# Performance work log

Measured on AMD Instinct MI355X. Metric: run time of the kernel, lower is better.

The kernel has to match this reference:

```python
import jax, jax.numpy as jnp
import numpy as np

B, N, T, D = 8, 32, 64, 128
E, H = 4, 32  # edge_dim, hidden_edge


def setup_inputs() -> dict:
    key = jax.random.key(0)
    ks = jax.random.split(key, 12)
    s = 1.0 / np.sqrt(D)
    inp = {
        "x": jax.random.normal(ks[0], (B, N, T, D), jnp.float32),
        "edge_features": jax.random.normal(ks[1], (B * T, N, N, E), jnp.float32),
        "A_prior": jax.random.uniform(ks[2], (B * T, N, N, 5), jnp.float32),
        "entity_padding_mask": jnp.zeros((B, N), bool),
        "Wq": jax.random.normal(ks[3], (D, D), jnp.float32) * s,
        "Wk": jax.random.normal(ks[4], (D, D), jnp.float32) * s,
        "Wv": jax.random.normal(ks[5], (D, D), jnp.float32) * s,
        "Theta": jax.random.normal(ks[6], (D, D), jnp.float32) * s,
        "W_fuse": jax.random.normal(ks[7], (1, 5), jnp.float32) * 0.4,
        "W1": jax.random.normal(ks[8], (H, 2 * D + E), jnp.float32) * (1.0 / np.sqrt(2 * D + E)),
        "b1": jnp.zeros((H,), jnp.float32),
        "W2": jax.random.normal(ks[9], (1, H), jnp.float32) * (1.0 / np.sqrt(H)),
        "b2": jnp.zeros((1,), jnp.float32),
        "gamma": jnp.ones((D,), jnp.float32),
        "beta": jnp.zeros((D,), jnp.float32),
        "phys_weight": jnp.array(1.0, jnp.float32),
        "prior_weight": jnp.array(1.0, jnp.float32),
    }
    return inp


def reference(x, edge_features, A_prior, entity_padding_mask, Wq, Wk, Wv, Theta,
              W_fuse, W1, b1, W2, b2, gamma, beta, phys_weight, prior_weight):
    b, n, t, d = x.shape
    BT = b * t
    Z = x.transpose(0, 2, 1, 3).reshape(BT, n, d)          # (BT, N, D)
    Q = Z @ Wq.T
    K = Z @ Wk.T
    V = Z @ Wv.T
    content = jnp.einsum('bnd,bmd->bnm', Q, K) / np.sqrt(d)
    # edge MLP: first linear decomposed over the concat [Qi, Kj, edge_features]
    W1q, W1k, W1e = W1[:, :d], W1[:, d:2 * d], W1[:, 2 * d:]
    hq = Q @ W1q.T                                          # (BT, N, H)
    hk = K @ W1k.T                                          # (BT, N, H)
    he = edge_features @ W1e.T                              # (BT, N, N, H)
    h = jax.nn.relu(hq[:, :, None, :] + hk[:, None, :, :] + he + b1)
    phys = (h @ W2.T)[..., 0] + b2[0]                       # (BT, N, N)
    logits = content + phys_weight * phys
    # prior fusion
    prior = (A_prior @ W_fuse.T)[..., 0]                    # (BT, N, N)
    prior = jnp.clip(jnp.nan_to_num(prior, nan=0.0, posinf=0.0, neginf=0.0), 0.0)
    logits = logits + prior_weight * jnp.log(prior + 1e-6)
    # padding mask
    mask_bt = jnp.broadcast_to(entity_padding_mask[:, None, :], (b, t, n)).reshape(BT, n)
    invalid = mask_bt[:, :, None] | mask_bt[:, None, :]
    logits = jnp.where(invalid, -1e9, logits)
    alpha = jax.nn.softmax(logits, axis=-1)
    spatial = jnp.einsum('bnm,bmd->bnd', alpha, V)
    out_f = (spatial @ Theta.T).reshape(b, t, n, d)
    y = Z.reshape(b, t, n, d) + out_f
    mu = y.mean(-1, keepdims=True)
    var = y.var(-1, keepdims=True)
    y = (y - mu) / jnp.sqrt(var + 1e-5) * gamma + beta      # LayerNorm
    out = y.transpose(0, 2, 1, 3)                           # (B, N, T, D)
    out = jnp.where(entity_padding_mask[:, :, None, None], 0.0, out)
    return out
```

## Files before the change

### kernel.cpp

```cpp
#include <hip/hip_runtime.h>


typedef __bf16 bf16x8 __attribute__((ext_vector_type(8)));
typedef float  f32x4  __attribute__((ext_vector_type(4)));

static __device__ __forceinline__ unsigned short f2bf(float f) {
    unsigned u = __float_as_uint(f);
    u += 0x7fffu + ((u >> 16) & 1u);
    return (unsigned short)(u >> 16);
}
static __device__ __forceinline__ float bf2f(unsigned short u) {
    return __uint_as_float(((unsigned)u) << 16);
}
static __device__ __forceinline__ unsigned pack2(float a, float b) {
    return (unsigned)f2bf(a) | ((unsigned)f2bf(b) << 16);
}


__global__ __launch_bounds__(256) void k0_prep(
    const float* __restrict__ Wq, const float* __restrict__ Wk,
    const float* __restrict__ Wv, const float* __restrict__ Theta,
    const float* __restrict__ W1, unsigned short* __restrict__ Wfrag)
{
    const int tid = threadIdx.x;
    if (blockIdx.x < 32) {
        int gid = blockIdx.x * 256 + tid;
        int g = gid >> 11, c = gid & 2047;
        int ntk = c >> 6, lane = c & 63;
        int i = (ntk >> 2) * 16 + (lane & 15);
        int j = (ntk & 3) * 32 + (lane >> 4) * 8;
        const float* src = (g == 0 ? Wq : g == 1 ? Wk : g == 2 ? Wv : Theta) + (size_t)i * 128 + j;
        float4 a = *(const float4*)(src);
        float4 b = *(const float4*)(src + 4);
        uint4 pk;
        pk.x = pack2(a.x, a.y); pk.y = pack2(a.z, a.w);
        pk.z = pack2(b.x, b.y); pk.w = pack2(b.z, b.w);
        *(uint4*)(Wfrag + (size_t)gid * 8) = pk;
    } else {
        int b2 = blockIdx.x - 32;
        int mat = b2 & 1;
        int hbase = (b2 >> 1) * 2;
        int hl = tid >> 7, col = tid & 127;
        int h = hbase + hl;
        const float* Wsel = mat ? Wk : Wq;
        const float* w1r = W1 + (size_t)h * 260 + mat * 128;
        float acc = 0.f;
        for (int i = 0; i < 128; ++i)
            acc = fmaf(w1r[i], Wsel[(size_t)i * 128 + col], acc);
        int nt = h >> 4;
        unsigned base = 65536u + (unsigned)mat * 4096u;
        int lane = (h & 15) | (((col >> 3) & 3) << 4);
        int ks = col >> 5, vj = col & 7;
        Wfrag[base + (unsigned)((nt * 4 + ks) * 64 + lane) * 8 + vj] = f2bf(acc);
    }
}

__global__ __launch_bounds__(256, 2)
void gnn_all(const float* __restrict__ x, const float* __restrict__ edge,
             const float* __restrict__ A_prior, const unsigned char* __restrict__ pad_mask,
             const unsigned short* __restrict__ Wfrag, const float* __restrict__ Wfuse,
             const float* __restrict__ W1, const float* __restrict__ b1,
             const float* __restrict__ W2, const float* __restrict__ b2,
             const float* __restrict__ gma, const float* __restrict__ bta,
             const float* __restrict__ physw, const float* __restrict__ priorw,
             float* __restrict__ out)
{
    __shared__ __align__(16) unsigned char arena[52224];
    float*          Qs    = (float*)arena;
    unsigned short* Zfrag = (unsigned short*)arena;
    float*          ThOut = Qs;
    float*          Ks    = (float*)(arena + 16896);
    unsigned short* Sfrag = (unsigned short*)(arena + 16896);
    unsigned short* Vs    = (unsigned short*)(arena + 33792);
    float*          Lg    = (float*)(arena + 42496);
    unsigned short* hqL   = (unsigned short*)(arena + 47104);
    unsigned short* hkL   = (unsigned short*)(arena + 49280);
    float4*         W1e_s = (float4*)(arena + 51456);
    float*          W2_s  = (float*)(arena + 51968);
    float*          maskrow = (float*)(arena + 52096);

    const int tid = threadIdx.x;
    const int bt  = blockIdx.x;
    const int b_  = bt >> 6, t_ = bt & 63;

    const float pw  = physw[0];
    const float rw_ = priorw[0];
    const float b2v = b2[0];
    const float wf0 = Wfuse[0], wf1 = Wfuse[1], wf2 = Wfuse[2],
                wf3 = Wfuse[3], wf4 = Wfuse[4];

    const int wv = tid >> 6, lane = tid & 63;
    const int quad = lane >> 4, col0 = lane & 15;
    const float b1lo = b1[col0], b1hi = b1[16 + col0];
    const int d0p = (tid & 31) * 4, ngp = tid >> 5;
    const float4 g4  = *(const float4*)(gma + d0p);
    const float4 be4 = *(const float4*)(bta + d0p);

    const int mp = tid & 15, npg = tid >> 4;
    const int n0 = npg * 2, mA = mp, mB = mp + 16;
    float4 e00, e01, e10, e11;
    float  prv00, prv01, prv10, prv11;
    {
        const size_t rowA0 = ((size_t)bt * 32 + n0) * 32;
        const size_t rowA1 = ((size_t)bt * 32 + n0 + 1) * 32;
        e00 = *(const float4*)(edge + (rowA0 + mA) * 4);
        e01 = *(const float4*)(edge + (rowA0 + mB) * 4);
        e10 = *(const float4*)(edge + (rowA1 + mA) * 4);
        e11 = *(const float4*)(edge + (rowA1 + mB) * 4);
        const float* p00 = A_prior + (rowA0 + mA) * 5;
        const float* p01 = A_prior + (rowA0 + mB) * 5;
        const float* p10 = A_prior + (rowA1 + mA) * 5;
        const float* p11 = A_prior + (rowA1 + mB) * 5;
        float q00 = p00[0]*wf0 + p00[1]*wf1 + p00[2]*wf2 + p00[3]*wf3 + p00[4]*wf4;
        float q01 = p01[0]*wf0 + p01[1]*wf1 + p01[2]*wf2 + p01[3]*wf3 + p01[4]*wf4;
        float q10 = p10[0]*wf0 + p10[1]*wf1 + p10[2]*wf2 + p10[3]*wf3 + p10[4]*wf4;
        float q11 = p11[0]*wf0 + p11[1]*wf1 + p11[2]*wf2 + p11[3]*wf3 + p11[4]*wf4;
        if (!(fabsf(q00) < 1e30f)) q00 = 0.f;
        if (!(fabsf(q01) < 1e30f)) q01 = 0.f;
        if (!(fabsf(q10) < 1e30f)) q10 = 0.f;
        if (!(fabsf(q11) < 1e30f)) q11 = 0.f;
        prv00 = rw_ * __logf(fmaxf(q00, 0.f) + 1e-6f);
        prv01 = rw_ * __logf(fmaxf(q01, 0.f) + 1e-6f);
        prv10 = rw_ * __logf(fmaxf(q10, 0.f) + 1e-6f);
        prv11 = rw_ * __logf(fmaxf(q11, 0.f) + 1e-6f);
    }

    if (tid < 32) {
        W1e_s[tid] = *(const float4*)(W1 + (size_t)tid * 260 + 256);
        W2_s[tid]  = W2[tid];
        maskrow[tid] = pad_mask[b_ * 32 + tid] ? 1.f : 0.f;
    }

#pragma unroll
    for (int it2 = 0; it2 < 2; ++it2) {
        int f = tid + 256 * it2;
        int lane9 = f & 63, tk = f >> 6;
        int nl = (tk >> 2) * 16 + (lane9 & 15);
        int d  = (tk & 3) * 32 + (lane9 >> 4) * 8;
        const float* xr = x + ((size_t)((b_ * 32 + nl) * 64 + t_)) * 128 + d;
        float4 a = *(const float4*)(xr);
        float4 b = *(const float4*)(xr + 4);
        uint4 pk;
        pk.x = pack2(a.x, a.y); pk.y = pack2(a.z, a.w);
        pk.z = pack2(b.x, b.y); pk.w = pack2(b.z, b.w);
        *(uint4*)(Zfrag + f * 8) = pk;
    }
    __syncthreads();

    bf16x8 az00 = *(const bf16x8*)(Zfrag + ((0 * 4 + 0) * 64 + lane) * 8);
    bf16x8 az01 = *(const bf16x8*)(Zfrag + ((0 * 4 + 1) * 64 + lane) * 8);
    bf16x8 az02 = *(const bf16x8*)(Zfrag + ((0 * 4 + 2) * 64 + lane) * 8);
    bf16x8 az03 = *(const bf16x8*)(Zfrag + ((0 * 4 + 3) * 64 + lane) * 8);
    bf16x8 az10 = *(const bf16x8*)(Zfrag + ((1 * 4 + 0) * 64 + lane) * 8);
    bf16x8 az11 = *(const bf16x8*)(Zfrag + ((1 * 4 + 1) * 64 + lane) * 8);
    bf16x8 az12 = *(const bf16x8*)(Zfrag + ((1 * 4 + 2) * 64 + lane) * 8);
    bf16x8 az13 = *(const bf16x8*)(Zfrag + ((1 * 4 + 3) * 64 + lane) * 8);
    __syncthreads();

    const bf16x8* WfG = (const bf16x8*)Wfrag;
    const f32x4 zero = {0.f, 0.f, 0.f, 0.f};

#pragma unroll
    for (int k7 = 0; k7 < 7; ++k7) {
        const int nt = wv + k7 * 4;
        const int cb = ((nt < 24) ? nt * 256 : 8192 + (nt - 24) * 256) + lane;
        bf16x8 bw0 = WfG[cb];
        bf16x8 bw1 = WfG[cb + 64];
        bf16x8 bw2 = WfG[cb + 128];
        bf16x8 bw3 = WfG[cb + 192];
        f32x4 acc0 = zero, acc1 = zero;
        acc0 = __builtin_amdgcn_mfma_f32_16x16x32_bf16(az00, bw0, acc0, 0, 0, 0);
        acc1 = __builtin_amdgcn_mfma_f32_16x16x32_bf16(az10, bw0, acc1, 0, 0, 0);
        acc0 = __builtin_amdgcn_mfma_f32_16x16x32_bf16(az01, bw1, acc0, 0, 0, 0);
        acc1 = __builtin_amdgcn_mfma_f32_16x16x32_bf16(az11, bw1, acc1, 0, 0, 0);
        acc0 = __builtin_amdgcn_mfma_f32_16x16x32_bf16(az02, bw2, acc0, 0, 0, 0);
        acc1 = __builtin_amdgcn_mfma_f32_16x16x32_bf16(az12, bw2, acc1, 0, 0, 0);
        acc0 = __builtin_amdgcn_mfma_f32_16x16x32_bf16(az03, bw3, acc0, 0, 0, 0);
        acc1 = __builtin_amdgcn_mfma_f32_16x16x32_bf16(az13, bw3, acc1, 0, 0, 0);
#pragma unroll
        for (int tg = 0; tg < 2; ++tg) {
            const f32x4 acc = tg ? acc1 : acc0;
            const int tokb = tg * 16 + quad * 4;
#pragma unroll
            for (int reg = 0; reg < 4; ++reg) {
                int tok = tokb + reg;
                float v = acc[reg];
                if (nt < 8)       Qs[tok * 132 + nt * 16 + col0] = v;
                else if (nt < 16) Ks[tok * 132 + (nt - 8) * 16 + col0] = v;
                else if (nt < 24) Vs[tok * 136 + (nt - 16) * 16 + col0] = f2bf(v);
                else if (nt < 26) hqL[tok * 34 + (nt - 24) * 16 + col0] = f2bf(v + (nt == 24 ? b1lo : b1hi));
                else              hkL[tok * 34 + (nt - 26) * 16 + col0] = f2bf(v);
            }
        }
    }
    __syncthreads();

    {
        const float* qa = Qs + n0 * 132;
        const float* qb = qa + 132;
        const float* ka = Ks + mA * 132;
        const float* kb = Ks + mB * 132;
        float a00 = 0.f, a01 = 0.f, a10 = 0.f, a11 = 0.f;
        for (int j = 0; j < 128; j += 4) {
            float4 kva = *(const float4*)(ka + j);
            float4 kvb = *(const float4*)(kb + j);
            float4 qva = *(const float4*)(qa + j);
            float4 qvb = *(const float4*)(qb + j);
            a00 = fmaf(qva.x, kva.x, fmaf(qva.y, kva.y, fmaf(qva.z, kva.z, fmaf(qva.w, kva.w, a00))));
            a01 = fmaf(qva.x, kvb.x, fmaf(qva.y, kvb.y, fmaf(qva.z, kvb.z, fmaf(qva.w, kvb.w, a01))));
            a10 = fmaf(qvb.x, kva.x, fmaf(qvb.y, kva.y, fmaf(qvb.z, kva.z, fmaf(qvb.w, kva.w, a10))));
            a11 = fmaf(qvb.x, kvb.x, fmaf(qvb.y, kvb.y, fmaf(qvb.z, kvb.z, fmaf(qvb.w, kvb.w, a11))));
        }
        float pc00 = 0.f, pc01 = 0.f, pc10 = 0.f, pc11 = 0.f;
#pragma unroll
        for (int h = 0; h < 32; ++h) {
            float4 we = W1e_s[h];
            float w2v = W2_s[h];
            float hq0 = bf2f(hqL[n0 * 34 + h]);
            float hq1 = bf2f(hqL[(n0 + 1) * 34 + h]);
            float hkA = bf2f(hkL[mA * 34 + h]);
            float hkB = bf2f(hkL[mB * 34 + h]);
            float heA0 = fmaf(e00.x, we.x, fmaf(e00.y, we.y, fmaf(e00.z, we.z, e00.w * we.w)));
            float heB0 = fmaf(e01.x, we.x, fmaf(e01.y, we.y, fmaf(e01.z, we.z, e01.w * we.w)));
            float heA1 = fmaf(e10.x, we.x, fmaf(e10.y, we.y, fmaf(e10.z, we.z, e10.w * we.w)));
            float heB1 = fmaf(e11.x, we.x, fmaf(e11.y, we.y, fmaf(e11.z, we.z, e11.w * we.w)));
            pc00 = fmaf(fmaxf(hq0 + hkA + heA0, 0.f), w2v, pc00);
            pc01 = fmaf(fmaxf(hq0 + hkB + heB0, 0.f), w2v, pc01);
            pc10 = fmaf(fmaxf(hq1 + hkA + heA1, 0.f), w2v, pc10);
            pc11 = fmaf(fmaxf(hq1 + hkB + heB1, 0.f), w2v, pc11);
        }
        const float SC = 0.08838834764831845f;
        float lg00 = a00 * SC + pw * (pc00 + b2v) + prv00;
        float lg01 = a01 * SC + pw * (pc01 + b2v) + prv01;
        float lg10 = a10 * SC + pw * (pc10 + b2v) + prv10;
        float lg11 = a11 * SC + pw * (pc11 + b2v) + prv11;
        float mr0 = maskrow[n0], mr1 = maskrow[n0 + 1];
        float mcA = maskrow[mA], mcB = maskrow[mB];
        if (mr0 != 0.f || mcA != 0.f) lg00 = -1e9f;
        if (mr0 != 0.f || mcB != 0.f) lg01 = -1e9f;
        if (mr1 != 0.f || mcA != 0.f) lg10 = -1e9f;
        if (mr1 != 0.f || mcB != 0.f) lg11 = -1e9f;
        {
            float mx = fmaxf(lg00, lg01);
#pragma unroll
            for (int off = 1; off < 16; off <<= 1)
                mx = fmaxf(mx, __shfl_xor(mx, off, 64));
            float ea = __expf(lg00 - mx);
            float eb = __expf(lg01 - mx);
            float s = ea + eb;
#pragma unroll
            for (int off = 1; off < 16; off <<= 1)
                s += __shfl_xor(s, off, 64);
            float inv = 1.f / s;
            Lg[n0 * 36 + mA] = ea * inv;
            Lg[n0 * 36 + mB] = eb * inv;
        }
        {
            float mx = fmaxf(lg10, lg11);
#pragma unroll
            for (int off = 1; off < 16; off <<= 1)
                mx = fmaxf(mx, __shfl_xor(mx, off, 64));
            float ea = __expf(lg10 - mx);
            float eb = __expf(lg11 - mx);
            float s = ea + eb;
#pragma unroll
            for (int off = 1; off < 16; off <<= 1)
                s += __shfl_xor(s, off, 64);
            float inv = 1.f / s;
            Lg[(n0 + 1) * 36 + mA] = ea * inv;
            Lg[(n0 + 1) * 36 + mB] = eb * inv;
        }
    }
    __syncthreads();

    const int rg = wv & 1, ch = wv >> 1;

    {
        const int vks = d0p >> 5, vq = (d0p >> 3) & 3, vj = d0p & 7;
        const int rb = ngp * 4;
        float s00=0.f,s01=0.f,s02=0.f,s03=0.f;
        float s10=0.f,s11=0.f,s12=0.f,s13=0.f;
        float s20=0.f,s21=0.f,s22=0.f,s23=0.f;
        float s30=0.f,s31=0.f,s32=0.f,s33=0.f;
        for (int m = 0; m < 32; m += 4) {
            float4 t0 = *(const float4*)(Lg + (rb + 0) * 36 + m);
            float4 t1 = *(const float4*)(Lg + (rb + 1) * 36 + m);
            float4 t2 = *(const float4*)(Lg + (rb + 2) * 36 + m);
            float4 t3 = *(const float4*)(Lg + (rb + 3) * 36 + m);
            uint2 w0 = *(const uint2*)(Vs + (m + 0) * 136 + d0p);
            uint2 w1 = *(const uint2*)(Vs + (m + 1) * 136 + d0p);
            uint2 w2 = *(const uint2*)(Vs + (m + 2) * 136 + d0p);
            uint2 w3 = *(const uint2*)(Vs + (m + 3) * 136 + d0p);
            {
                float v0 = bf2f((unsigned short)(w0.x & 0xffffu));
                float v1 = bf2f((unsigned short)(w0.x >> 16));
                float v2 = bf2f((unsigned short)(w0.y & 0xffffu));
                float v3 = bf2f((unsigned short)(w0.y >> 16));
                s00=fmaf(t0.x,v0,s00); s01=fmaf(t0.x,v1,s01); s02=fmaf(t0.x,v2,s02); s03=fmaf(t0.x,v3,s03);
                s10=fmaf(t1.x,v0,s10); s11=fmaf(t1.x,v1,s11); s12=fmaf(t1.x,v2,s12); s13=fmaf(t1.x,v3,s13);
                s20=fmaf(t2.x,v0,s20); s21=fmaf(t2.x,v1,s21); s22=fmaf(t2.x,v2,s22); s23=fmaf(t2.x,v3,s23);
                s30=fmaf(t3.x,v0,s30); s31=fmaf(t3.x,v1,s31); s32=fmaf(t3.x,v2,s32); s33=fmaf(t3.x,v3,s33);
            }
            {
                float v0 = bf2f((unsigned short)(w1.x & 0xffffu));
                float v1 = bf2f((unsigned short)(w1.x >> 16));
                float v2 = bf2f((unsigned short)(w1.y & 0xffffu));
                float v3 = bf2f((unsigned short)(w1.y >> 16));
                s00=fmaf(t0.y,v0,s00); s01=fmaf(t0.y,v1,s01); s02=fmaf(t0.y,v2,s02); s03=fmaf(t0.y,v3,s03);
                s10=fmaf(t1.y,v0,s10); s11=fmaf(t1.y,v1,s11); s12=fmaf(t1.y,v2,s12); s13=fmaf(t1.y,v3,s13);
                s20=fmaf(t2.y,v0,s20); s21=fmaf(t2.y,v1,s21); s22=fmaf(t2.y,v2,s22); s23=fmaf(t2.y,v3,s23);
                s30=fmaf(t3.y,v0,s30); s31=fmaf(t3.y,v1,s31); s32=fmaf(t3.y,v2,s32); s33=fmaf(t3.y,v3,s33);
            }
            {
                float v0 = bf2f((unsigned short)(w2.x & 0xffffu));
                float v1 = bf2f((unsigned short)(w2.x >> 16));
                float v2 = bf2f((unsigned short)(w2.y & 0xffffu));
                float v3 = bf2f((unsigned short)(w2.y >> 16));
                s00=fmaf(t0.z,v0,s00); s01=fmaf(t0.z,v1,s01); s02=fmaf(t0.z,v2,s02); s03=fmaf(t0.z,v3,s03);
                s10=fmaf(t1.z,v0,s10); s11=fmaf(t1.z,v1,s11); s12=fmaf(t1.z,v2,s12); s13=fmaf(t1.z,v3,s13);
                s20=fmaf(t2.z,v0,s20); s21=fmaf(t2.z,v1,s21); s22=fmaf(t2.z,v2,s22); s23=fmaf(t2.z,v3,s23);
                s30=fmaf(t3.z,v0,s30); s31=fmaf(t3.z,v1,s31); s32=fmaf(t3.z,v2,s32); s33=fmaf(t3.z,v3,s33);
            }
            {
                float v0 = bf2f((unsigned short)(w3.x & 0xffffu));
                float v1 = bf2f((unsigned short)(w3.x >> 16));
                float v2 = bf2f((unsigned short)(w3.y & 0xffffu));
                float v3 = bf2f((unsigned short)(w3.y >> 16));
                s00=fmaf(t0.w,v0,s00); s01=fmaf(t0.w,v1,s01); s02=fmaf(t0.w,v2,s02); s03=fmaf(t0.w,v3,s03);
                s10=fmaf(t1.w,v0,s10); s11=fmaf(t1.w,v1,s11); s12=fmaf(t1.w,v2,s12); s13=fmaf(t1.w,v3,s13);
                s20=fmaf(t2.w,v0,s20); s21=fmaf(t2.w,v1,s21); s22=fmaf(t2.w,v2,s22); s23=fmaf(t2.w,v3,s23);
                s30=fmaf(t3.w,v0,s30); s31=fmaf(t3.w,v1,s31); s32=fmaf(t3.w,v2,s32); s33=fmaf(t3.w,v3,s33);
            }
        }
        {
            int nloc = rb + 0; int tg = nloc >> 4, nl = nloc & 15;
            unsigned short* sp = Sfrag + ((tg * 4 + vks) * 64 + vq * 16 + nl) * 8 + vj;
            sp[0] = f2bf(s00); sp[1] = f2bf(s01); sp[2] = f2bf(s02); sp[3] = f2bf(s03);
        }
        {
            int nloc = rb + 1; int tg = nloc >> 4, nl = nloc & 15;
            unsigned short* sp = Sfrag + ((tg * 4 + vks) * 64 + vq * 16 + nl) * 8 + vj;
            sp[0] = f2bf(s10); sp[1] = f2bf(s11); sp[2] = f2bf(s12); sp[3] = f2bf(s13);
        }
        {
            int nloc = rb + 2; int tg = nloc >> 4, nl = nloc & 15;
            unsigned short* sp = Sfrag + ((tg * 4 + vks) * 64 + vq * 16 + nl) * 8 + vj;
            sp[0] = f2bf(s20); sp[1] = f2bf(s21); sp[2] = f2bf(s22); sp[3] = f2bf(s23);
        }
        {
            int nloc = rb + 3; int tg = nloc >> 4, nl = nloc & 15;
            unsigned short* sp = Sfrag + ((tg * 4 + vks) * 64 + vq * 16 + nl) * 8 + vj;
            sp[0] = f2bf(s30); sp[1] = f2bf(s31); sp[2] = f2bf(s32); sp[3] = f2bf(s33);
        }
    }
    __syncthreads();

    {
        f32x4 aT0 = zero, aT1 = zero, aT2 = zero, aT3 = zero;
        bf16x8 av0 = *(const bf16x8*)(Sfrag + ((rg * 4 + 0) * 64 + lane) * 8);
        bf16x8 av1 = *(const bf16x8*)(Sfrag + ((rg * 4 + 1) * 64 + lane) * 8);
        bf16x8 av2 = *(const bf16x8*)(Sfrag + ((rg * 4 + 2) * 64 + lane) * 8);
        bf16x8 av3 = *(const bf16x8*)(Sfrag + ((rg * 4 + 3) * 64 + lane) * 8);
        {
            const int cb = 6144 + ((ch * 4 + 0) * 4) * 64 + lane;
            aT0 = __builtin_amdgcn_mfma_f32_16x16x32_bf16(av0, WfG[cb], aT0, 0, 0, 0);
            aT0 = __builtin_amdgcn_mfma_f32_16x16x32_bf16(av1, WfG[cb + 64], aT0, 0, 0, 0);
            aT0 = __builtin_amdgcn_mfma_f32_16x16x32_bf16(av2, WfG[cb + 128], aT0, 0, 0, 0);
            aT0 = __builtin_amdgcn_mfma_f32_16x16x32_bf16(av3, WfG[cb + 192], aT0, 0, 0, 0);
        }
        {
            const int cb = 6144 + ((ch * 4 + 1) * 4) * 64 + lane;
            aT1 = __builtin_amdgcn_mfma_f32_16x16x32_bf16(av0, WfG[cb], aT1, 0, 0, 0);
            aT1 = __builtin_amdgcn_mfma_f32_16x16x32_bf16(av1, WfG[cb + 64], aT1, 0, 0, 0);
            aT1 = __builtin_amdgcn_mfma_f32_16x16x32_bf16(av2, WfG[cb + 128], aT1, 0, 0, 0);
            aT1 = __builtin_amdgcn_mfma_f32_16x16x32_bf16(av3, WfG[cb + 192], aT1, 0, 0, 0);
        }
        {
            const int cb = 6144 + ((ch * 4 + 2) * 4) * 64 + lane;
            aT2 = __builtin_amdgcn_mfma_f32_16x16x32_bf16(av0, WfG[cb], aT2, 0, 0, 0);
            aT2 = __builtin_amdgcn_mfma_f32_16x16x32_bf16(av1, WfG[cb + 64], aT2, 0, 0, 0);
            aT2 = __builtin_amdgcn_mfma_f32_16x16x32_bf16(av2, WfG[cb + 128], aT2, 0, 0, 0);
            aT2 = __builtin_amdgcn_mfma_f32_16x16x32_bf16(av3, WfG[cb + 192], aT2, 0, 0, 0);
        }
        {
            const int cb = 6144 + ((ch * 4 + 3) * 4) * 64 + lane;
            aT3 = __builtin_amdgcn_mfma_f32_16x16x32_bf16(av0, WfG[cb], aT3, 0, 0, 0);
            aT3 = __builtin_amdgcn_mfma_f32_16x16x32_bf16(av1, WfG[cb + 64], aT3, 0, 0, 0);
            aT3 = __builtin_amdgcn_mfma_f32_16x16x32_bf16(av2, WfG[cb + 128], aT3, 0, 0, 0);
            aT3 = __builtin_amdgcn_mfma_f32_16x16x32_bf16(av3, WfG[cb + 192], aT3, 0, 0, 0);
        }
        const int rbase = rg * 16 + quad * 4;
#pragma unroll
        for (int reg = 0; reg < 4; ++reg) {
            ThOut[(rbase + reg) * 132 + ch * 64 + 0  * 16 + col0] = aT0[reg];
            ThOut[(rbase + reg) * 132 + ch * 64 + 1  * 16 + col0] = aT1[reg];
            ThOut[(rbase + reg) * 132 + ch * 64 + 2  * 16 + col0] = aT2[reg];
            ThOut[(rbase + reg) * 132 + ch * 64 + 3  * 16 + col0] = aT3[reg];
        }
    }
    __syncthreads();

    {
#pragma unroll
        for (int r = 0; r < 4; ++r) {
            int nloc = ngp * 4 + r;
            const float* xr = x + ((size_t)((b_ * 32 + nloc) * 64 + t_)) * 128 + d0p;
            float4 z  = *(const float4*)(xr);
            float4 th = *(const float4*)(ThOut + nloc * 132 + d0p);
            float y0 = th.x + z.x, y1 = th.y + z.y, y2 = th.z + z.z, y3 = th.w + z.w;
            float s  = (y0 + y1) + (y2 + y3);
            float s2 = (y0*y0 + y1*y1) + (y2*y2 + y3*y3);
#pragma unroll
            for (int off = 1; off < 32; off <<= 1) {
                s  += __shfl_xor(s,  off, 64);
                s2 += __shfl_xor(s2, off, 64);
            }
            float mu   = s * 0.0078125f;
            float var  = s2 * 0.0078125f - mu * mu;
            float rstd = rsqrtf(var + 1e-5f);
            float msk  = (maskrow[nloc] != 0.f) ? 0.f : 1.f;
            float4 o;
            o.x = ((y0 - mu) * rstd * g4.x + be4.x) * msk;
            o.y = ((y1 - mu) * rstd * g4.y + be4.y) * msk;
            o.z = ((y2 - mu) * rstd * g4.z + be4.z) * msk;
            o.w = ((y3 - mu) * rstd * g4.w + be4.w) * msk;
            *(float4*)(out + ((size_t)((b_ * 32 + nloc) * 64 + t_)) * 128 + d0p) = o;
        }
    }
}

extern "C" void kernel_launch(void* const* d_in, const int* in_sizes, int n_in,
                              void* d_out, int out_size, void* d_ws, size_t ws_size,
                              hipStream_t stream) {
    const float* x        = (const float*)d_in[0];
    const float* edge     = (const float*)d_in[1];
    const float* A_prior  = (const float*)d_in[2];
    const unsigned char* pad_mask = (const unsigned char*)d_in[3];
    const float* Wq       = (const float*)d_in[4];
    const float* Wk       = (const float*)d_in[5];
    const float* Wv       = (const float*)d_in[6];
    const float* Theta    = (const float*)d_in[7];
    const float* Wfuse    = (const float*)d_in[8];
    const float* W1       = (const float*)d_in[9];
    const float* b1       = (const float*)d_in[10];
    const float* W2       = (const float*)d_in[11];
    const float* b2       = (const float*)d_in[12];
    const float* gma      = (const float*)d_in[13];
    const float* bta      = (const float*)d_in[14];
    const float* physw    = (const float*)d_in[15];
    const float* priorw   = (const float*)d_in[16];
    float* out = (float*)d_out;

    unsigned short* Wfrag = (unsigned short*)d_ws;

    k0_prep<<<dim3(64), dim3(256), 0, stream>>>(Wq, Wk, Wv, Theta, W1, Wfrag);
    gnn_all<<<dim3(512), dim3(256), 0, stream>>>(
        x, edge, A_prior, pad_mask, Wfrag, Wfuse,
        W1, b1, W2, b2, gma, bta, physw, priorw, out);
}
```

Before: 126.2 us.

## Fold Theta into value projection and drop the output MFMA stage

The prep kernel now computes the product Theta·Wv and stores it in bf16 fragment form in the slot previously used for Wv. The main kernel's V projection therefore already includes Theta, so the separate Theta MFMA stage, its shared-memory staging and two block barriers are removed. The attention-weighted sum then feeds LayerNorm directly, with the residual x rows prefetched before that loop. The edge-MLP loop also reads hq/hk as packed 32-bit pairs instead of single bf16 values. In exchange the prep kernel runs extra serial 128-length dot products, and rounding the combined weight matrix to bf16 slightly changes numerics.

```diff
diff --git a/kernel.cpp b/kernel.cpp
--- a/kernel.cpp
+++ b/kernel.cpp
@@ -23,21 +23,22 @@
     const float* __restrict__ W1, unsigned short* __restrict__ Wfrag)
 {
     const int tid = threadIdx.x;
-    if (blockIdx.x < 32) {
-        int gid = blockIdx.x * 256 + tid;
+    const int blk = blockIdx.x;
+    if (blk < 16) {
+        int gid = blk * 256 + tid;
         int g = gid >> 11, c = gid & 2047;
         int ntk = c >> 6, lane = c & 63;
         int i = (ntk >> 2) * 16 + (lane & 15);
         int j = (ntk & 3) * 32 + (lane >> 4) * 8;
-        const float* src = (g == 0 ? Wq : g == 1 ? Wk : g == 2 ? Wv : Theta) + (size_t)i * 128 + j;
+        const float* src = (g == 0 ? Wq : Wk) + (size_t)i * 128 + j;
         float4 a = *(const float4*)(src);
         float4 b = *(const float4*)(src + 4);
         uint4 pk;
         pk.x = pack2(a.x, a.y); pk.y = pack2(a.z, a.w);
         pk.z = pack2(b.x, b.y); pk.w = pack2(b.z, b.w);
         *(uint4*)(Wfrag + (size_t)gid * 8) = pk;
-    } else {
-        int b2 = blockIdx.x - 32;
+    } else if (blk < 48) {
+        int b2 = blk - 16;
         int mat = b2 & 1;
         int hbase = (b2 >> 1) * 2;
         int hl = tid >> 7, col = tid & 127;
@@ -52,6 +53,29 @@
         int lane = (h & 15) | (((col >> 3) & 3) << 4);
         int ks = col >> 5, vj = col & 7;
         Wfrag[base + (unsigned)((nt * 4 + ks) * 64 + lane) * 8 + vj] = f2bf(acc);
+    } else {
+        int b2 = blk - 48;
+        int i  = b2 * 4 + (tid >> 6);
+        int j0 = (tid & 63) * 2;
+        const float* trow = Theta + (size_t)i * 128;
+        float m0 = 0.f, m1 = 0.f;
+        for (int k = 0; k < 128; ++k) {
+            float tv = trow[k];
+            m0 = fmaf(tv, Wv[(size_t)k * 128 + j0], m0);
+            m1 = fmaf(tv, Wv[(size_t)k * 128 + j0 + 1], m1);
+        }
+        {
+            int jj = j0;
+            int ntk = (i >> 4) * 4 + (jj >> 5);
+            int lane = (i & 15) | (((jj >> 3) & 3) << 4);
+            Wfrag[(unsigned)((4096 + ntk * 64 + lane) * 8 + (jj & 7))] = f2bf(m0);
+        }
+        {
+            int jj = j0 + 1;
+            int ntk = (i >> 4) * 4 + (jj >> 5);
+            int lane = (i & 15) | (((jj >> 3) & 3) << 4);
+            Wfrag[(unsigned)((4096 + ntk * 64 + lane) * 8 + (jj & 7))] = f2bf(m1);
+        }
     }
 }
 
@@ -68,9 +92,7 @@
     __shared__ __align__(16) unsigned char arena[52224];
     float*          Qs    = (float*)arena;
     unsigned short* Zfrag = (unsigned short*)arena;
-    float*          ThOut = Qs;
     float*          Ks    = (float*)(arena + 16896);
-    unsigned short* Sfrag = (unsigned short*)(arena + 16896);
     unsigned short* Vs    = (unsigned short*)(arena + 33792);
     float*          Lg    = (float*)(arena + 42496);
     unsigned short* hqL   = (unsigned short*)(arena + 47104);
@@ -211,23 +233,33 @@
             a10 = fmaf(qvb.x, kva.x, fmaf(qvb.y, kva.y, fmaf(qvb.z, kva.z, fmaf(qvb.w, kva.w, a10))));
             a11 = fmaf(qvb.x, kvb.x, fmaf(qvb.y, kvb.y, fmaf(qvb.z, kvb.z, fmaf(qvb.w, kvb.w, a11))));
         }
+        const unsigned* hq0p = (const unsigned*)(hqL + n0 * 34);
+        const unsigned* hq1p = (const unsigned*)(hqL + (n0 + 1) * 34);
+        const unsigned* hkAp = (const unsigned*)(hkL + mA * 34);
+        const unsigned* hkBp = (const unsigned*)(hkL + mB * 34);
         float pc00 = 0.f, pc01 = 0.f, pc10 = 0.f, pc11 = 0.f;
 #pragma unroll
-        for (int h = 0; h < 32; ++h) {
-            float4 we = W1e_s[h];
-            float w2v = W2_s[h];
-            float hq0 = bf2f(hqL[n0 * 34 + h]);
-            float hq1 = bf2f(hqL[(n0 + 1) * 34 + h]);
-            float hkA = bf2f(hkL[mA * 34 + h]);
-            float hkB = bf2f(hkL[mB * 34 + h]);
-            float heA0 = fmaf(e00.x, we.x, fmaf(e00.y, we.y, fmaf(e00.z, we.z, e00.w * we.w)));
-            float heB0 = fmaf(e01.x, we.x, fmaf(e01.y, we.y, fmaf(e01.z, we.z, e01.w * we.w)));
-            float heA1 = fmaf(e10.x, we.x, fmaf(e10.y, we.y, fmaf(e10.z, we.z, e10.w * we.w)));
-            float heB1 = fmaf(e11.x, we.x, fmaf(e11.y, we.y, fmaf(e11.z, we.z, e11.w * we.w)));
-            pc00 = fmaf(fmaxf(hq0 + hkA + heA0, 0.f), w2v, pc00);
-            pc01 = fmaf(fmaxf(hq0 + hkB + heB0, 0.f), w2v, pc01);
-            pc10 = fmaf(fmaxf(hq1 + hkA + heA1, 0.f), w2v, pc10);
-            pc11 = fmaf(fmaxf(hq1 + hkB + heB1, 0.f), w2v, pc11);
+        for (int h2 = 0; h2 < 16; ++h2) {
+            unsigned uq0 = hq0p[h2], uq1 = hq1p[h2];
+            unsigned ukA = hkAp[h2], ukB = hkBp[h2];
+#pragma unroll
+            for (int hb = 0; hb < 2; ++hb) {
+                int h = h2 * 2 + hb;
+                float4 we = W1e_s[h];
+                float w2v = W2_s[h];
+                float hq0 = bf2f((unsigned short)(hb ? (uq0 >> 16) : (uq0 & 0xffffu)));
+                float hq1 = bf2f((unsigned short)(hb ? (uq1 >> 16) : (uq1 & 0xffffu)));
+                float hkA = bf2f((unsigned short)(hb ? (ukA >> 16) : (ukA & 0xffffu)));
+                float hkB = bf2f((unsigned short)(hb ? (ukB >> 16) : (ukB & 0xffffu)));
+                float heA0 = fmaf(e00.x, we.x, fmaf(e00.y, we.y, fmaf(e00.z, we.z, e00.w * we.w)));
+                float heB0 = fmaf(e01.x, we.x, fmaf(e01.y, we.y, fmaf(e01.z, we.z, e01.w * we.w)));
+                float heA1 = fmaf(e10.x, we.x, fmaf(e10.y, we.y, fmaf(e10.z, we.z, e10.w * we.w)));
+                float heB1 = fmaf(e11.x, we.x, fmaf(e11.y, we.y, fmaf(e11.z, we.z, e11.w * we.w)));
+                pc00 = fmaf(fmaxf(hq0 + hkA + heA0, 0.f), w2v, pc00);
+                pc01 = fmaf(fmaxf(hq0 + hkB + heB0, 0.f), w2v, pc01);
+                pc10 = fmaf(fmaxf(hq1 + hkA + heA1, 0.f), w2v, pc10);
+                pc11 = fmaf(fmaxf(hq1 + hkB + heB1, 0.f), w2v, pc11);
+            }
         }
         const float SC = 0.08838834764831845f;
         float lg00 = a00 * SC + pw * (pc00 + b2v) + prv00;
@@ -273,11 +305,13 @@
     }
     __syncthreads();
 
-    const int rg = wv & 1, ch = wv >> 1;
-
     {
-        const int vks = d0p >> 5, vq = (d0p >> 3) & 3, vj = d0p & 7;
         const int rb = ngp * 4;
+        float4 xp0 = *(const float4*)(x + ((size_t)((b_ * 32 + rb + 0) * 64 + t_)) * 128 + d0p);
+        float4 xp1 = *(const float4*)(x + ((size_t)((b_ * 32 + rb + 1) * 64 + t_)) * 128 + d0p);
+        float4 xp2 = *(const float4*)(x + ((size_t)((b_ * 32 + rb + 2) * 64 + t_)) * 128 + d0p);
+        float4 xp3 = *(const float4*)(x + ((size_t)((b_ * 32 + rb + 3) * 64 + t_)) * 128 + d0p);
+
         float s00=0.f,s01=0.f,s02=0.f,s03=0.f;
         float s10=0.f,s11=0.f,s12=0.f,s13=0.f;
         float s20=0.f,s21=0.f,s22=0.f,s23=0.f;
@@ -332,99 +366,70 @@
                 s30=fmaf(t3.w,v0,s30); s31=fmaf(t3.w,v1,s31); s32=fmaf(t3.w,v2,s32); s33=fmaf(t3.w,v3,s33);
             }
         }
-        {
-            int nloc = rb + 0; int tg = nloc >> 4, nl = nloc & 15;
-            unsigned short* sp = Sfrag + ((tg * 4 + vks) * 64 + vq * 16 + nl) * 8 + vj;
-            sp[0] = f2bf(s00); sp[1] = f2bf(s01); sp[2] = f2bf(s02); sp[3] = f2bf(s03);
-        }
-        {
-            int nloc = rb + 1; int tg = nloc >> 4, nl = nloc & 15;
-            unsigned short* sp = Sfrag + ((tg * 4 + vks) * 64 + vq * 16 + nl) * 8 + vj;
-            sp[0] = f2bf(s10); sp[1] = f2bf(s11); sp[2] = f2bf(s12); sp[3] = f2bf(s13);
-        }
-        {
-            int nloc = rb + 2; int tg = nloc >> 4, nl = nloc & 15;
-            unsigned short* sp = Sfrag + ((tg * 4 + vks) * 64 + vq * 16 + nl) * 8 + vj;
-            sp[0] = f2bf(s20); sp[1] = f2bf(s21); sp[2] = f2bf(s22); sp[3] = f2bf(s23);
-        }
-        {
-            int nloc = rb + 3; int tg = nloc >> 4, nl = nloc & 15;
-            unsigned short* sp = Sfrag + ((tg * 4 + vks) * 64 + vq * 16 + nl) * 8 + vj;
-            sp[0] = f2bf(s30); sp[1] = f2bf(s31); sp[2] = f2bf(s32); sp[3] = f2bf(s33);
-        }
-    }
-    __syncthreads();
-
-    {
-        f32x4 aT0 = zero, aT1 = zero, aT2 = zero, aT3 = zero;
-        bf16x8 av0 = *(const bf16x8*)(Sfrag + ((rg * 4 + 0) * 64 + lane) * 8);
-        bf16x8 av1 = *(const bf16x8*)(Sfrag + ((rg * 4 + 1) * 64 + lane) * 8);
-        bf16x8 av2 = *(const bf16x8*)(Sfrag + ((rg * 4 + 2) * 64 + lane) * 8);
-        bf16x8 av3 = *(const bf16x8*)(Sfrag + ((rg * 4 + 3) * 64 + lane) * 8);
-        {
-            const int cb = 6144 + ((ch * 4 + 0) * 4) * 64 + lane;
-            aT0 = __builtin_amdgcn_mfma_f32_16x16x32_bf16(av0, WfG[cb], aT0, 0, 0, 0);
-            aT0 = __builtin_amdgcn_mfma_f32_16x16x32_bf16(av1, WfG[cb + 64], aT0, 0, 0, 0);
-            aT0 = __builtin_amdgcn_mfma_f32_16x16x32_bf16(av2, WfG[cb + 128], aT0, 0, 0, 0);
-            aT0 = __builtin_amdgcn_mfma_f32_16x16x32_bf16(av3, WfG[cb + 192], aT0, 0, 0, 0);
-        }
-        {
-            const int cb = 6144 + ((ch * 4 + 1) * 4) * 64 + lane;
-            aT1 = __builtin_amdgcn_mfma_f32_16x16x32_bf16(av0, WfG[cb], aT1, 0, 0, 0);
-            aT1 = __builtin_amdgcn_mfma_f32_16x16x32_bf16(av1, WfG[cb + 64], aT1, 0, 0, 0);
-            aT1 = __builtin_amdgcn_mfma_f32_16x16x32_bf16(av2, WfG[cb + 128], aT1, 0, 0, 0);
-            aT1 = __builtin_amdgcn_mfma_f32_16x16x32_bf16(av3, WfG[cb + 192], aT1, 0, 0, 0);
-        }
-        {
-            const int cb = 6144 + ((ch * 4 + 2) * 4) * 64 + lane;
-            aT2 = __builtin_amdgcn_mfma_f32_16x16x32_bf16(av0, WfG[cb], aT2, 0, 0, 0);
-            aT2 = __builtin_amdgcn_mfma_f32_16x16x32_bf16(av1, WfG[cb + 64], aT2, 0, 0, 0);
-            aT2 = __builtin_amdgcn_mfma_f32_16x16x32_bf16(av2, WfG[cb + 128], aT2, 0, 0, 0);
-            aT2 = __builtin_amdgcn_mfma_f32_16x16x32_bf16(av3, WfG[cb + 192], aT2, 0, 0, 0);
-        }
-        {
-            const int cb = 6144 + ((ch * 4 + 3) * 4) * 64 + lane;
-            aT3 = __builtin_amdgcn_mfma_f32_16x16x32_bf16(av0, WfG[cb], aT3, 0, 0, 0);
-            aT3 = __builtin_amdgcn_mfma_f32_16x16x32_bf16(av1, WfG[cb + 64], aT3, 0, 0, 0);
-            aT3 = __builtin_amdgcn_mfma_f32_16x16x32_bf16(av2, WfG[cb + 128], aT3, 0, 0, 0);
-            aT3 = __builtin_amdgcn_mfma_f32_16x16x32_bf16(av3, WfG[cb + 192], aT3, 0, 0, 0);
-        }
-        const int rbase = rg * 16 + quad * 4;
-#pragma unroll
-        for (int reg = 0; reg < 4; ++reg) {
-            ThOut[(rbase + reg) * 132 + ch * 64 + 0  * 16 + col0] = aT0[reg];
-            ThOut[(rbase + reg) * 132 + ch * 64 + 1  * 16 + col0] = aT1[reg];
-            ThOut[(rbase + reg) * 132 + ch * 64 + 2  * 16 + col0] = aT2[reg];
-            ThOut[(rbase + reg) * 132 + ch * 64 + 3  * 16 + col0] = aT3[reg];
-        }
-    }
-    __syncthreads();
-
-    {
-#pragma unroll
-        for (int r = 0; r < 4; ++r) {
-            int nloc = ngp * 4 + r;
-            const float* xr = x + ((size_t)((b_ * 32 + nloc) * 64 + t_)) * 128 + d0p;
-            float4 z  = *(const float4*)(xr);
-            float4 th = *(const float4*)(ThOut + nloc * 132 + d0p);
-            float y0 = th.x + z.x, y1 = th.y + z.y, y2 = th.z + z.z, y3 = th.w + z.w;
+
+        {
+            float y0 = s00 + xp0.x, y1 = s01 + xp0.y, y2 = s02 + xp0.z, y3 = s03 + xp0.w;
             float s  = (y0 + y1) + (y2 + y3);
             float s2 = (y0*y0 + y1*y1) + (y2*y2 + y3*y3);
 #pragma unroll
-            for (int off = 1; off < 32; off <<= 1) {
-                s  += __shfl_xor(s,  off, 64);
-                s2 += __shfl_xor(s2, off, 64);
-            }
-            float mu   = s * 0.0078125f;
-            float var  = s2 * 0.0078125f - mu * mu;
+            for (int off = 1; off < 32; off <<= 1) { s += __shfl_xor(s, off, 64); s2 += __shfl_xor(s2, off, 64); }
+            float mu = s * 0.0078125f, var = s2 * 0.0078125f - mu * mu;
             float rstd = rsqrtf(var + 1e-5f);
-            float msk  = (maskrow[nloc] != 0.f) ? 0.f : 1.f;
+            float msk = (maskrow[rb + 0] != 0.f) ? 0.f : 1.f;
             float4 o;
             o.x = ((y0 - mu) * rstd * g4.x + be4.x) * msk;
             o.y = ((y1 - mu) * rstd * g4.y + be4.y) * msk;
             o.z = ((y2 - mu) * rstd * g4.z + be4.z) * msk;
             o.w = ((y3 - mu) * rstd * g4.w + be4.w) * msk;
-            *(float4*)(out + ((size_t)((b_ * 32 + nloc) * 64 + t_)) * 128 + d0p) = o;
+            *(float4*)(out + ((size_t)((b_ * 32 + rb + 0) * 64 + t_)) * 128 + d0p) = o;
+        }
+        {
+            float y0 = s10 + xp1.x, y1 = s11 + xp1.y, y2 = s12 + xp1.z, y3 = s13 + xp1.w;
+            float s  = (y0 + y1) + (y2 + y3);
+            float s2 = (y0*y0 + y1*y1) + (y2*y2 + y3*y3);
+#pragma unroll
+            for (int off = 1; off < 32; off <<= 1) { s += __shfl_xor(s, off, 64); s2 += __shfl_xor(s2, off, 64); }
+            float mu = s * 0.0078125f, var = s2 * 0.0078125f - mu * mu;
+            float rstd = rsqrtf(var + 1e-5f);
+            float msk = (maskrow[rb + 1] != 0.f) ? 0.f : 1.f;
+            float4 o;
+            o.x = ((y0 - mu) * rstd * g4.x + be4.x) * msk;
+            o.y = ((y1 - mu) * rstd * g4.y + be4.y) * msk;
+            o.z = ((y2 - mu) * rstd * g4.z + be4.z) * msk;
+            o.w = ((y3 - mu) * rstd * g4.w + be4.w) * msk;
+            *(float4*)(out + ((size_t)((b_ * 32 + rb + 1) * 64 + t_)) * 128 + d0p) = o;
+        }
+        {
+            float y0 = s20 + xp2.x, y1 = s21 + xp2.y, y2 = s22 + xp2.z, y3 = s23 + xp2.w;
+            float s  = (y0 + y1) + (y2 + y3);
+            float s2 = (y0*y0 + y1*y1) + (y2*y2 + y3*y3);
+#pragma unroll
+            for (int off = 1; off < 32; off <<= 1) { s += __shfl_xor(s, off, 64); s2 += __shfl_xor(s2, off, 64); }
+            float mu = s * 0.0078125f, var = s2 * 0.0078125f - mu * mu;
+            float rstd = rsqrtf(var + 1e-5f);
+            float msk = (maskrow[rb + 2] != 0.f) ? 0.f : 1.f;
+            float4 o;
+            o.x = ((y0 - mu) * rstd * g4.x + be4.x) * msk;
+            o.y = ((y1 - mu) * rstd * g4.y + be4.y) * msk;
+            o.z = ((y2 - mu) * rstd * g4.z + be4.z) * msk;
+            o.w = ((y3 - mu) * rstd * g4.w + be4.w) * msk;
+            *(float4*)(out + ((size_t)((b_ * 32 + rb + 2) * 64 + t_)) * 128 + d0p) = o;
+        }
+        {
+            float y0 = s30 + xp3.x, y1 = s31 + xp3.y, y2 = s32 + xp3.z, y3 = s33 + xp3.w;
+            float s  = (y0 + y1) + (y2 + y3);
+            float s2 = (y0*y0 + y1*y1) + (y2*y2 + y3*y3);
+#pragma unroll
+            for (int off = 1; off < 32; off <<= 1) { s += __shfl_xor(s, off, 64); s2 += __shfl_xor(s2, off, 64); }
+            float mu = s * 0.0078125f, var = s2 * 0.0078125f - mu * mu;
+            float rstd = rsqrtf(var + 1e-5f);
+            float msk = (maskrow[rb + 3] != 0.f) ? 0.f : 1.f;
+            float4 o;
+            o.x = ((y0 - mu) * rstd * g4.x + be4.x) * msk;
+            o.y = ((y1 - mu) * rstd * g4.y + be4.y) * msk;
+            o.z = ((y2 - mu) * rstd * g4.z + be4.z) * msk;
+            o.w = ((y3 - mu) * rstd * g4.w + be4.w) * msk;
+            *(float4*)(out + ((size_t)((b_ * 32 + rb + 3) * 64 + t_)) * 128 + d0p) = o;
         }
     }
 }
@@ -453,7 +458,7 @@
 
     unsigned short* Wfrag = (unsigned short*)d_ws;
 
-    k0_prep<<<dim3(64), dim3(256), 0, stream>>>(Wq, Wk, Wv, Theta, W1, Wfrag);
+    k0_prep<<<dim3(80), dim3(256), 0, stream>>>(Wq, Wk, Wv, Theta, W1, Wfrag);
     gnn_all<<<dim3(512), dim3(256), 0, stream>>>(
         x, edge, A_prior, pad_mask, Wfrag, Wfuse,
         W1, b1, W2, b2, gma, bta, physw, priorw, out);
```

Measured after the change: 125.9 us. No clear change (-0.3%).
